# Performance work log

Measured on AMD Instinct MI355X. Metric: run time of the kernel, lower is better.

The kernel has to match this reference:

```python
import jax, jax.numpy as jnp
import numpy as np

N_DEPTH = 16  # == serialization_depth init kwarg


def _normalize(v, axis):
    # F.normalize: v / max(||v||, 1e-12)
    return v / jnp.maximum(jnp.linalg.norm(v, axis=axis, keepdims=True), 1e-12)


def _weighted_mean(p, mask):
    # p: [B,N,1], mask: [B,N]
    n = jnp.sum(mask, axis=1, keepdims=True)[..., None]
    return jnp.sum(p * mask[..., None], axis=1, keepdims=True) / (n + 1e-9)


def _select_duplet(points, m, k1, k2):
    # pick 2 random valid points (argmin of rand + big penalty on masked-out) and average
    B, N, _ = points.shape
    def pick(k):
        s = jax.random.uniform(k, (B, N)) + (1.0 - m) * 1e9
        idx = jnp.argmin(s, axis=1)           # [B]
        return jnp.take_along_axis(points, idx[:, None, None], axis=1)  # [B,1,3]
    return (pick(k1) + pick(k2)) * 0.5


def _align(points, ml, mr, ks):
    pl = points - _select_duplet(points, ml, ks[0], ks[1])
    pr = points - _select_duplet(points, mr, ks[2], ks[3])
    return pl * ml[..., None] + pr * mr[..., None]


def _serialize(coords, mask, n_depth, key):
    B, N, _ = coords.shape
    inf = float(2 ** (n_depth // 2 + 3))
    s0 = 2 ** (n_depth // 2 + 1)
    # integer halving each step, exactly like score_scale // 2 in torch
    scales = jnp.asarray(np.array([s0 >> i for i in range(n_depth)], dtype=np.float32))
    keys = jax.random.split(key, n_depth * 5).reshape(n_depth, 5)

    total0 = jnp.zeros((B, N, 1), coords.dtype)
    oldABC0 = jnp.ones((B, 3, 1), coords.dtype)

    def step(carry, inp):
        points, oldABC, total = carry
        ks, scale = inp
        ABC = jax.random.normal(ks[0], (B, 3, 1), coords.dtype)
        angle = jnp.sum(_normalize(ABC, 1) * _normalize(oldABC, 1), axis=1, keepdims=True)
        sgn = jnp.sign(angle)
        sgn = jnp.where(sgn == 0, 1.0, sgn)
        ABC = ABC * sgn
        proj = points @ ABC                    # [B,N,1]
        proj = proj - _weighted_mean(proj, mask)
        score = jnp.sign(proj)                 # [B,N,1]
        total = total + score * scale
        ml = jnp.minimum(jax.nn.relu(-score[..., 0]), mask)
        mr = jnp.minimum(jax.nn.relu(score[..., 0]), mask)
        points = _align(points, ml, mr, ks[1:])
        return (points, ABC, total), None

    (_, _, total), _ = jax.lax.scan(step, (coords, oldABC0, total0), (keys, scales))
    total = total + inf * (1.0 - mask)[..., None]
    return jnp.argsort(total[..., 0], axis=1)  # [B,N]


def setup_inputs() -> dict:
    key = jax.random.key(0)
    k1, k2 = jax.random.split(key)
    B, N, D = 16, 8192, 256
    x = jax.random.normal(k1, (B, N, D), dtype=jnp.float32)
    x_coords = jax.random.normal(k2, (B, N, 3), dtype=jnp.float32)
    mask = jnp.ones((B, N), dtype=jnp.float32)
    return {"x": x, "x_coords": x_coords, "mask": mask}


def reference(x, x_coords, mask):
    key = jax.random.key(42)
    idx = _serialize(x_coords, mask, N_DEPTH, key)   # [B,N] int
    # reverse_indices: gather(arange, idx) == idx, then argsort
    rev = jnp.argsort(idx, axis=1)
    x_out = jnp.take_along_axis(x, idx[:, :, None], axis=1)
    return x_out, rev
```

## Files before the change

kernel.cpp:

```cpp
#include <hip/hip_runtime.h>
#include <stdint.h>

#pragma clang fp contract(off)

constexpr bool kPartitionable = true;

constexpr int B_ = 16;
constexpr int N_ = 8192;
constexpr int TPB = 1024;

__device__ __forceinline__ void tf2x32(uint32_t k0, uint32_t k1,
                                       uint32_t x0, uint32_t x1,
                                       uint32_t& o0, uint32_t& o1) {
  uint32_t ks2 = k0 ^ k1 ^ 0x1BD11BDAu;
  x0 += k0; x1 += k1;
#define RND(r) { x0 += x1; x1 = (x1 << (r)) | (x1 >> (32 - (r))); x1 ^= x0; }
  RND(13) RND(15) RND(26) RND(6)   x0 += k1;  x1 += ks2 + 1u;
  RND(17) RND(29) RND(16) RND(24)  x0 += ks2; x1 += k0  + 2u;
  RND(13) RND(15) RND(26) RND(6)   x0 += k0;  x1 += k1  + 3u;
  RND(17) RND(29) RND(16) RND(24)  x0 += k1;  x1 += ks2 + 4u;
  RND(13) RND(15) RND(26) RND(6)   x0 += ks2; x1 += k0  + 5u;
#undef RND
  o0 = x0; o1 = x1;
}

__device__ __forceinline__ uint32_t rbits(uint32_t k0, uint32_t k1,
                                          uint32_t i, uint32_t half) {
  uint32_t o0, o1;
  if (kPartitionable) {
    tf2x32(k0, k1, 0u, i, o0, o1);
    return o0 ^ o1;
  } else {
    if (i < half) { tf2x32(k0, k1, i, half + i, o0, o1); return o0; }
    else          { tf2x32(k0, k1, i - half, i, o0, o1); return o1; }
  }
}

__device__ __forceinline__ void derive_key(uint32_t j, uint32_t& k0, uint32_t& k1) {
  uint32_t o0, o1;
  if (kPartitionable) {
    tf2x32(0u, 42u, 0u, j, o0, o1);
    k0 = o0; k1 = o1;
  } else {
    uint32_t a = 2u * j, b = 2u * j + 1u, t0, t1;
    if (a < 80u) { tf2x32(0u, 42u, a, 80u + a, t0, t1); k0 = t0; }
    else         { tf2x32(0u, 42u, a - 80u, a, t0, t1); k0 = t1; }
    if (b < 80u) { tf2x32(0u, 42u, b, 80u + b, t0, t1); k1 = t0; }
    else         { tf2x32(0u, 42u, b - 80u, b, t0, t1); k1 = t1; }
  }
}

__device__ __forceinline__ float u01_from_bits(uint32_t bits) {
  return __fsub_rn(__uint_as_float((bits >> 9) | 0x3f800000u), 1.0f);
}

__device__ __forceinline__ float xla_logf(float x) {
  uint32_t ix = __float_as_uint(x);
  int e = (int)((ix >> 23) & 0xffu) - 126;
  float m = __uint_as_float((ix & 0x007fffffu) | 0x3f000000u);
  float ef = (float)e;
  if (m < 0.707106781186547524f) {
    ef = __fsub_rn(ef, 1.0f);
    m = __fsub_rn(__fadd_rn(m, m), 1.0f);
  } else {
    m = __fsub_rn(m, 1.0f);
  }
  float z = __fmul_rn(m, m);
  float y = 7.0376836292e-2f;
  y = __fadd_rn(__fmul_rn(y, m), -1.1514610310e-1f);
  y = __fadd_rn(__fmul_rn(y, m),  1.1676998740e-1f);
  y = __fadd_rn(__fmul_rn(y, m), -1.2420140846e-1f);
  y = __fadd_rn(__fmul_rn(y, m),  1.4249322787e-1f);
  y = __fadd_rn(__fmul_rn(y, m), -1.6668057665e-1f);
  y = __fadd_rn(__fmul_rn(y, m),  2.0000714765e-1f);
  y = __fadd_rn(__fmul_rn(y, m), -2.4999993993e-1f);
  y = __fadd_rn(__fmul_rn(y, m),  3.3333331174e-1f);
  y = __fmul_rn(__fmul_rn(y, m), z);
  y = __fadd_rn(y, __fmul_rn(ef, -2.12194440e-4f));
  y = __fadd_rn(y, __fmul_rn(-0.5f, z));
  float r = __fadd_rn(m, y);
  r = __fadd_rn(r, __fmul_rn(ef, 0.693359375f));
  return r;
}

__device__ __forceinline__ float xla_log1p(float z) {
  if (fabsf(z) < 1e-4f)
    return __fmul_rn(__fadd_rn(__fmul_rn(-0.5f, z), 1.0f), z);
  return xla_logf(__fadd_rn(z, 1.0f));
}

__device__ __forceinline__ float erfinv_xla(float x) {
  float xx = __fmul_rn(x, x);
  float w = -xla_log1p(-xx);
  float p;
  if (w < 5.0f) {
    float ww = __fsub_rn(w, 2.5f);
    p = 2.81022636e-08f;
    p = __fadd_rn(__fmul_rn(p, ww),  3.43273939e-07f);
    p = __fadd_rn(__fmul_rn(p, ww), -3.5233877e-06f);
    p = __fadd_rn(__fmul_rn(p, ww), -4.39150654e-06f);
    p = __fadd_rn(__fmul_rn(p, ww),  0.00021858087f);
    p = __fadd_rn(__fmul_rn(p, ww), -0.00125372503f);
    p = __fadd_rn(__fmul_rn(p, ww), -0.00417768164f);
    p = __fadd_rn(__fmul_rn(p, ww),  0.246640727f);
    p = __fadd_rn(__fmul_rn(p, ww),  1.50140941f);
  } else {
    float ww = __fsub_rn(__fsqrt_rn(w), 3.0f);
    p = -0.000200214257f;
    p = __fadd_rn(__fmul_rn(p, ww),  0.000100950558f);
    p = __fadd_rn(__fmul_rn(p, ww),  0.00134934322f);
    p = __fadd_rn(__fmul_rn(p, ww), -0.00367342844f);
    p = __fadd_rn(__fmul_rn(p, ww),  0.00573950773f);
    p = __fadd_rn(__fmul_rn(p, ww), -0.0076224613f);
    p = __fadd_rn(__fmul_rn(p, ww),  0.00943887047f);
    p = __fadd_rn(__fmul_rn(p, ww),  1.00167406f);
    p = __fadd_rn(__fmul_rn(p, ww),  2.83297682f);
  }
  return __fmul_rn(p, x);
}

#define ACC4(v) { s = __fadd_rn(s, (v).x); s = __fadd_rn(s, (v).y); \
                  s = __fadd_rn(s, (v).z); s = __fadd_rn(s, (v).w); }

__device__ __forceinline__ float seq_sum_8192(const float4* v) {
  float4 a0=v[0],a1=v[1],a2=v[2],a3=v[3],a4=v[4],a5=v[5],a6=v[6],a7=v[7];
  float s = 0.f;
  for (int c = 0; c < 256; c += 2) {
    const int nb = (c + 1) << 3, na = (c + 2) << 3;
    float4 b0=v[nb+0],b1=v[nb+1],b2=v[nb+2],b3=v[nb+3];
    float4 b4=v[nb+4],b5=v[nb+5],b6=v[nb+6],b7=v[nb+7];
    ACC4(a0) ACC4(a1) ACC4(a2) ACC4(a3) ACC4(a4) ACC4(a5) ACC4(a6) ACC4(a7)
    a0=v[na+0];a1=v[na+1];a2=v[na+2];a3=v[na+3];
    a4=v[na+4];a5=v[na+5];a6=v[na+6];a7=v[na+7];
    ACC4(b0) ACC4(b1) ACC4(b2) ACC4(b3) ACC4(b4) ACC4(b5) ACC4(b6) ACC4(b7)
  }
  return s;
}

__global__ __launch_bounds__(TPB, 1)
void serialize_kernel(const float* __restrict__ coords, const float* __restrict__ mask,
                      float* __restrict__ pts_ws, int* __restrict__ idx_ws,
                      float* __restrict__ rev_out) {
  const int b = blockIdx.x;
  const int tid = threadIdx.x;

  __shared__ __align__(16) float pm[N_ + 32];
  __shared__ float    pv[4][16];
  __shared__ int      pi[4][16];
  __shared__ float    s_abcs[10][3], s_dl[3], s_dr[3];
  __shared__ float    s_stash[32];
  __shared__ float    s_mean, s_denom;
  __shared__ uint32_t s_k0[50], s_k1[50];

  float* pts = pts_ws + (size_t)b * N_ * 3;
  const float* cb = coords + (size_t)b * N_ * 3;
  const float* mb = mask + (size_t)b * N_;

  const float kLo = -0x1.fffffep-1f;
  const float kSqrt2 = 0x1.6a09e6p+0f;

  if (tid < 50) derive_key((uint32_t)tid, s_k0[tid], s_k1[tid]);

  float m_[8];
  {
    float4 m4a = *(const float4*)(mb + 4 * tid);
    float4 m4b = *(const float4*)(mb + 4096 + 4 * tid);
    m_[0]=m4a.x; m_[1]=m4a.y; m_[2]=m4a.z; m_[3]=m4a.w;
    m_[4]=m4b.x; m_[5]=m4b.y; m_[6]=m4b.z; m_[7]=m4b.w;
    ((float4*)pm)[tid] = m4a;
    ((float4*)pm)[1024 + tid] = m4b;
  }

  float p_[8][3];
  {
    const float4* cA = (const float4*)(cb + 12 * tid);
    const float4* cB = (const float4*)(cb + 12288 + 12 * tid);
    float4 v0=cA[0], v1=cA[1], v2=cA[2];
    p_[0][0]=v0.x; p_[0][1]=v0.y; p_[0][2]=v0.z;
    p_[1][0]=v0.w; p_[1][1]=v1.x; p_[1][2]=v1.y;
    p_[2][0]=v1.z; p_[2][1]=v1.w; p_[2][2]=v2.x;
    p_[3][0]=v2.y; p_[3][1]=v2.z; p_[3][2]=v2.w;
    float4 w0=cB[0], w1=cB[1], w2=cB[2];
    p_[4][0]=w0.x; p_[4][1]=w0.y; p_[4][2]=w0.z;
    p_[5][0]=w0.w; p_[5][1]=w1.x; p_[5][2]=w1.y;
    p_[6][0]=w1.z; p_[6][1]=w1.w; p_[6][2]=w2.x;
    p_[7][0]=w2.y; p_[7][1]=w2.z; p_[7][2]=w2.w;
    float4* dA = (float4*)(pts + 12 * tid);
    float4* dB = (float4*)(pts + 12288 + 12 * tid);
    dA[0]=v0; dA[1]=v1; dA[2]=v2;
    dB[0]=w0; dB[1]=w1; dB[2]=w2;
  }

  float tot_[8];
#pragma unroll
  for (int e = 0; e < 8; ++e) tot_[e] = 0.f;

  __syncthreads();

  if (tid == 0) {
    __builtin_amdgcn_s_setprio(1);
    float s = seq_sum_8192((const float4*)pm);
    __builtin_amdgcn_s_setprio(0);
    s_denom = __fadd_rn(s, 1e-9f);
  } else if (tid == 64) {
    float o0 = 1.f, o1 = 1.f, o2 = 1.f;
    for (int tt = 0; tt < 10; ++tt) {
      float a[3];
#pragma unroll
      for (int c = 0; c < 3; ++c) {
        uint32_t bits = rbits(s_k0[5*tt], s_k1[5*tt], (uint32_t)(b*3 + c), 24u);
        float f = u01_from_bits(bits);
        float u = __fadd_rn(__fmul_rn(f, 2.0f), kLo);
        u = fmaxf(kLo, u);
        a[c] = __fmul_rn(kSqrt2, erfinv_xla(u));
      }
      float na2 = __fadd_rn(__fadd_rn(__fmul_rn(a[0],a[0]),__fmul_rn(a[1],a[1])),__fmul_rn(a[2],a[2]));
      float no2 = __fadd_rn(__fadd_rn(__fmul_rn(o0,o0),__fmul_rn(o1,o1)),__fmul_rn(o2,o2));
      float nan_ = fmaxf(__fsqrt_rn(na2), 1e-12f);
      float non_ = fmaxf(__fsqrt_rn(no2), 1e-12f);
      float u0=__fdiv_rn(a[0],nan_), u1=__fdiv_rn(a[1],nan_), u2=__fdiv_rn(a[2],nan_);
      float v0=__fdiv_rn(o0,non_),  v1=__fdiv_rn(o1,non_),  v2=__fdiv_rn(o2,non_);
      float ang = __fadd_rn(__fadd_rn(__fmul_rn(u0,v0),__fmul_rn(u1,v1)),__fmul_rn(u2,v2));
      float sg = (ang > 0.f) ? 1.f : ((ang < 0.f) ? -1.f : 1.f);
      a[0]=__fmul_rn(a[0],sg); a[1]=__fmul_rn(a[1],sg); a[2]=__fmul_rn(a[2],sg);
      s_abcs[tt][0]=a[0]; s_abcs[tt][1]=a[1]; s_abcs[tt][2]=a[2];
      o0=a[0]; o1=a[1]; o2=a[2];
    }
  }
  __syncthreads();

  float proj_[8], sc_[8];

  for (int t = 0; t < 10; ++t) {
    const float A0 = s_abcs[t][0], A1 = s_abcs[t][1], A2 = s_abcs[t][2];

#pragma unroll
    for (int e = 0; e < 8; ++e)
      proj_[e] = __fadd_rn(__fadd_rn(__fmul_rn(p_[e][0], A0), __fmul_rn(p_[e][1], A1)),
                           __fmul_rn(p_[e][2], A2));
    {
      float4 w0, w1;
      w0.x=__fmul_rn(proj_[0],m_[0]); w0.y=__fmul_rn(proj_[1],m_[1]);
      w0.z=__fmul_rn(proj_[2],m_[2]); w0.w=__fmul_rn(proj_[3],m_[3]);
      w1.x=__fmul_rn(proj_[4],m_[4]); w1.y=__fmul_rn(proj_[5],m_[5]);
      w1.z=__fmul_rn(proj_[6],m_[6]); w1.w=__fmul_rn(proj_[7],m_[7]);
      ((float4*)pm)[tid] = w0;
      ((float4*)pm)[1024 + tid] = w1;
    }
    __syncthreads();

    if (tid == 0) {
#pragma unroll
      for (int e = 0; e < 8; ++e) {
        s_stash[e*3+0]=p_[e][0]; s_stash[e*3+1]=p_[e][1]; s_stash[e*3+2]=p_[e][2];
        s_stash[24+e]=tot_[e];
      }
      __builtin_amdgcn_s_setprio(1);
      float s = seq_sum_8192((const float4*)pm);
      __builtin_amdgcn_s_setprio(0);
      s_mean = __fdiv_rn(s, s_denom);
#pragma unroll
      for (int e = 0; e < 8; ++e) {
        p_[e][0]=s_stash[e*3+0]; p_[e][1]=s_stash[e*3+1]; p_[e][2]=s_stash[e*3+2];
        tot_[e]=s_stash[24+e];
      }
    }

    float f_[4][8];
#pragma unroll
    for (int q = 0; q < 4; ++q) {
      uint32_t kk0 = s_k0[5*t+1+q], kk1 = s_k1[5*t+1+q];
#pragma unroll
      for (int e = 0; e < 8; ++e) {
        int n = (e < 4) ? (4*tid + e) : (4096 + 4*tid + (e - 4));
        f_[q][e] = u01_from_bits(rbits(kk0, kk1, (uint32_t)(b*N_ + n), 65536u));
      }
    }
    __syncthreads();

    const float mean = s_mean;
    const float sca = (float)(512u >> t);
    float bv[4]; int bi_[4];
#pragma unroll
    for (int q = 0; q < 4; ++q) { bv[q] = 1e30f; bi_[q] = 0x7fffffff; }
#pragma unroll
    for (int e = 0; e < 8; ++e) {
      float d = __fsub_rn(proj_[e], mean);
      float s0 = (d > 0.f) ? 1.f : ((d < 0.f) ? -1.f : 0.f);
      sc_[e] = s0;
      tot_[e] = __fadd_rn(tot_[e], __fmul_rn(s0, sca));
      float mlv = fminf(fmaxf(-s0, 0.f), m_[e]);
      float mrv = fminf(fmaxf( s0, 0.f), m_[e]);
      int n = (e < 4) ? (4*tid + e) : (4096 + 4*tid + (e - 4));
#pragma unroll
      for (int q = 0; q < 4; ++q) {
        float meff = (q < 2) ? mlv : mrv;
        float val = __fadd_rn(f_[q][e], __fmul_rn(__fsub_rn(1.0f, meff), 1e9f));
        if (val < bv[q] || (val == bv[q] && n < bi_[q])) { bv[q] = val; bi_[q] = n; }
      }
    }
#pragma unroll
    for (int off = 32; off > 0; off >>= 1) {
#pragma unroll
      for (int q = 0; q < 4; ++q) {
        float vv = __shfl_xor(bv[q], off);
        int   ii = __shfl_xor(bi_[q], off);
        if (vv < bv[q] || (vv == bv[q] && ii < bi_[q])) { bv[q] = vv; bi_[q] = ii; }
      }
    }
    if ((tid & 63) == 0) {
      int w = tid >> 6;
#pragma unroll
      for (int q = 0; q < 4; ++q) { pv[q][w] = bv[q]; pi[q][w] = bi_[q]; }
    }
    __syncthreads();

    if (tid < 64) {
      int w = tid & 15, q = tid >> 4;
      float v = pv[q][w]; int i = pi[q][w];
#pragma unroll
      for (int off = 1; off < 16; off <<= 1) {
        float vv = __shfl_xor(v, off);
        int   ii = __shfl_xor(i, off);
        if (vv < v || (vv == v && ii < i)) { v = vv; i = ii; }
      }
      int g0 = __shfl(i, 0), g1 = __shfl(i, 16), g2 = __shfl(i, 32), g3 = __shfl(i, 48);
      if (tid == 0) {
#pragma unroll
        for (int c = 0; c < 3; ++c) {
          s_dl[c] = __fmul_rn(__fadd_rn(pts[g0*3+c], pts[g1*3+c]), 0.5f);
          s_dr[c] = __fmul_rn(__fadd_rn(pts[g2*3+c], pts[g3*3+c]), 0.5f);
        }
      }
    }
    __syncthreads();

    {
      float dl0=s_dl[0], dl1=s_dl[1], dl2=s_dl[2];
      float dr0=s_dr[0], dr1=s_dr[1], dr2=s_dr[2];
#pragma unroll
      for (int e = 0; e < 8; ++e) {
        float s0 = sc_[e];
        float mlv = fminf(fmaxf(-s0, 0.f), m_[e]);
        float mrv = fminf(fmaxf( s0, 0.f), m_[e]);
        p_[e][0] = __fadd_rn(__fmul_rn(__fsub_rn(p_[e][0], dl0), mlv),
                             __fmul_rn(__fsub_rn(p_[e][0], dr0), mrv));
        p_[e][1] = __fadd_rn(__fmul_rn(__fsub_rn(p_[e][1], dl1), mlv),
                             __fmul_rn(__fsub_rn(p_[e][1], dr1), mrv));
        p_[e][2] = __fadd_rn(__fmul_rn(__fsub_rn(p_[e][2], dl2), mlv),
                             __fmul_rn(__fsub_rn(p_[e][2], dr2), mrv));
      }
      float4 v0, v1, v2;
      v0.x=p_[0][0]; v0.y=p_[0][1]; v0.z=p_[0][2]; v0.w=p_[1][0];
      v1.x=p_[1][1]; v1.y=p_[1][2]; v1.z=p_[2][0]; v1.w=p_[2][1];
      v2.x=p_[2][2]; v2.y=p_[3][0]; v2.z=p_[3][1]; v2.w=p_[3][2];
      float4* dA = (float4*)(pts + 12 * tid);
      dA[0]=v0; dA[1]=v1; dA[2]=v2;
      v0.x=p_[4][0]; v0.y=p_[4][1]; v0.z=p_[4][2]; v0.w=p_[5][0];
      v1.x=p_[5][1]; v1.y=p_[5][2]; v1.z=p_[6][0]; v1.w=p_[6][1];
      v2.x=p_[6][2]; v2.y=p_[7][0]; v2.z=p_[7][1]; v2.w=p_[7][2];
      float4* dB = (float4*)(pts + 12288 + 12 * tid);
      dB[0]=v0; dB[1]=v1; dB[2]=v2;
    }
  }

  uint32_t* keys = reinterpret_cast<uint32_t*>(pm);
  {
    uint32_t kk_[8];
#pragma unroll
    for (int e = 0; e < 8; ++e) {
      int n = (e < 4) ? (4*tid + e) : (4096 + 4*tid + (e - 4));
      float tf = __fadd_rn(tot_[e], __fmul_rn(2048.0f, __fsub_rn(1.0f, m_[e])));
      int bin = (int)tf + 1023;
      bin = min(max(bin, 0), 4095);
      kk_[e] = ((uint32_t)bin << 13) | (uint32_t)n;
    }
    uint4 u0, u1;
    u0.x=kk_[0]; u0.y=kk_[1]; u0.z=kk_[2]; u0.w=kk_[3];
    u1.x=kk_[4]; u1.y=kk_[5]; u1.z=kk_[6]; u1.w=kk_[7];
    ((uint4*)keys)[tid] = u0;
    ((uint4*)keys)[1024 + tid] = u1;
  }
  for (uint32_t kk = 2; kk <= (uint32_t)N_; kk <<= 1) {
    for (uint32_t j = kk >> 1; j > 0; j >>= 1) {
      __syncthreads();
#pragma unroll
      for (int r = 0; r < 4; ++r) {
        int pidx = tid + (r << 10);
        int i = ((pidx & ~((int)j - 1)) << 1) | (pidx & ((int)j - 1));
        int l = i | (int)j;
        uint32_t a = keys[i], c2 = keys[l];
        bool up = ((i & (int)kk) == 0);
        if ((a > c2) == up) { keys[i] = c2; keys[l] = a; }
      }
    }
  }
  __syncthreads();
#pragma unroll
  for (int r = 0; r < 8; ++r) {
    int pos = tid + (r << 10);
    uint32_t key = keys[pos];
    int n = (int)(key & 8191u);
    idx_ws[b * N_ + pos] = n;
    rev_out[b * N_ + n] = (float)pos;
  }
}

__global__ __launch_bounds__(256)
void gather_kernel(const float* __restrict__ x, const int* __restrict__ idx_ws,
                   float* __restrict__ out) {
  int row = blockIdx.x * 4 + (threadIdx.x >> 6);
  int lane = threadIdx.x & 63;
  int b = row >> 13;
  int n = idx_ws[row];
  const float4* src = reinterpret_cast<const float4*>(x + ((size_t)(b * N_ + n)) * 256);
  float4* dst = reinterpret_cast<float4*>(out + (size_t)row * 256);
  dst[lane] = src[lane];
}

extern "C" void kernel_launch(void* const* d_in, const int* in_sizes, int n_in,
                              void* d_out, int out_size, void* d_ws, size_t ws_size,
                              hipStream_t stream) {
  const float* x      = (const float*)d_in[0];
  const float* coords = (const float*)d_in[1];
  const float* mask   = (const float*)d_in[2];
  float* out = (float*)d_out;
  float* pts_ws = (float*)d_ws;
  int*   idx_ws = (int*)((char*)d_ws + (size_t)B_ * N_ * 3 * sizeof(float));
  float* rev_out = out + (size_t)B_ * N_ * 256;

  serialize_kernel<<<dim3(B_), dim3(TPB), 0, stream>>>(coords, mask, pts_ws, idx_ws, rev_out);
  gather_kernel<<<dim3(B_ * N_ / 4), dim3(256), 0, stream>>>(x, idx_ws, out);
}
```

Before: 635.5 us.

## Precompute random uniforms and ABC vectors in a separate wide kernel

Moves the Threefry random generation for the argmin selection and the ABC direction vectors out of the 16-block serialize kernel into a new 641-block kernel, which writes them to workspace for serialize to load. This spreads the heavy hash work across the whole GPU instead of 16 CUs inside the serial loop. The mask denominator is now computed with a wave-shuffle reduction instead of a sequential single-thread sum. In exchange it adds a kernel launch and about 20 MB of global write plus read traffic. The parallel denominator sum may round differently from the sequential order used before.

```diff
diff --git a/kernel.cpp b/kernel.cpp
--- a/kernel.cpp
+++ b/kernel.cpp
@@ -8,6 +8,7 @@
 constexpr int B_ = 16;
 constexpr int N_ = 8192;
 constexpr int TPB = 1024;
+constexpr int NSTEP = 10;
 
 __device__ __forceinline__ void tf2x32(uint32_t k0, uint32_t k1,
                                        uint32_t x0, uint32_t x1,
@@ -24,30 +25,16 @@
   o0 = x0; o1 = x1;
 }
 
-__device__ __forceinline__ uint32_t rbits(uint32_t k0, uint32_t k1,
-                                          uint32_t i, uint32_t half) {
+__device__ __forceinline__ uint32_t rbits(uint32_t k0, uint32_t k1, uint32_t i) {
   uint32_t o0, o1;
-  if (kPartitionable) {
-    tf2x32(k0, k1, 0u, i, o0, o1);
-    return o0 ^ o1;
-  } else {
-    if (i < half) { tf2x32(k0, k1, i, half + i, o0, o1); return o0; }
-    else          { tf2x32(k0, k1, i - half, i, o0, o1); return o1; }
-  }
+  tf2x32(k0, k1, 0u, i, o0, o1);
+  return o0 ^ o1;
 }
 
 __device__ __forceinline__ void derive_key(uint32_t j, uint32_t& k0, uint32_t& k1) {
   uint32_t o0, o1;
-  if (kPartitionable) {
-    tf2x32(0u, 42u, 0u, j, o0, o1);
-    k0 = o0; k1 = o1;
-  } else {
-    uint32_t a = 2u * j, b = 2u * j + 1u, t0, t1;
-    if (a < 80u) { tf2x32(0u, 42u, a, 80u + a, t0, t1); k0 = t0; }
-    else         { tf2x32(0u, 42u, a - 80u, a, t0, t1); k0 = t1; }
-    if (b < 80u) { tf2x32(0u, 42u, b, 80u + b, t0, t1); k1 = t0; }
-    else         { tf2x32(0u, 42u, b - 80u, b, t0, t1); k1 = t1; }
-  }
+  tf2x32(0u, 42u, 0u, j, o0, o1);
+  k0 = o0; k1 = o1;
 }
 
 __device__ __forceinline__ float u01_from_bits(uint32_t bits) {
@@ -119,6 +106,60 @@
   return __fmul_rn(p, x);
 }
 
+__global__ __launch_bounds__(TPB)
+void rand_kernel(float* __restrict__ uni, float* __restrict__ abc) {
+  const int blk = blockIdx.x;
+  const int tid = threadIdx.x;
+  if (blk < 640) {
+    int b = blk / 40, r = blk % 40, t = r / 4, q = r % 4;
+    uint32_t k0, k1;
+    derive_key((uint32_t)(5 * t + 1 + q), k0, k1);
+    float* dst = uni + (((size_t)b * NSTEP + t) * 4 + q) * (size_t)N_;
+    float4 lo, hi;
+    int n0 = 4 * tid, n1 = 4096 + 4 * tid;
+    lo.x = u01_from_bits(rbits(k0, k1, (uint32_t)(b * N_ + n0 + 0)));
+    lo.y = u01_from_bits(rbits(k0, k1, (uint32_t)(b * N_ + n0 + 1)));
+    lo.z = u01_from_bits(rbits(k0, k1, (uint32_t)(b * N_ + n0 + 2)));
+    lo.w = u01_from_bits(rbits(k0, k1, (uint32_t)(b * N_ + n0 + 3)));
+    hi.x = u01_from_bits(rbits(k0, k1, (uint32_t)(b * N_ + n1 + 0)));
+    hi.y = u01_from_bits(rbits(k0, k1, (uint32_t)(b * N_ + n1 + 1)));
+    hi.z = u01_from_bits(rbits(k0, k1, (uint32_t)(b * N_ + n1 + 2)));
+    hi.w = u01_from_bits(rbits(k0, k1, (uint32_t)(b * N_ + n1 + 3)));
+    *(float4*)(dst + n0) = lo;
+    *(float4*)(dst + n1) = hi;
+  } else if (tid < 16) {
+    const int b = tid;
+    const float kLo = -0x1.fffffep-1f;
+    const float kSqrt2 = 0x1.6a09e6p+0f;
+    float o0 = 1.f, o1 = 1.f, o2 = 1.f;
+    for (int t = 0; t < NSTEP; ++t) {
+      uint32_t k0, k1;
+      derive_key((uint32_t)(5 * t), k0, k1);
+      float a[3];
+#pragma unroll
+      for (int c = 0; c < 3; ++c) {
+        float f = u01_from_bits(rbits(k0, k1, (uint32_t)(b * 3 + c)));
+        float u = __fadd_rn(__fmul_rn(f, 2.0f), kLo);
+        u = fmaxf(kLo, u);
+        a[c] = __fmul_rn(kSqrt2, erfinv_xla(u));
+      }
+      float na2 = __fadd_rn(__fadd_rn(__fmul_rn(a[0],a[0]),__fmul_rn(a[1],a[1])),__fmul_rn(a[2],a[2]));
+      float no2 = __fadd_rn(__fadd_rn(__fmul_rn(o0,o0),__fmul_rn(o1,o1)),__fmul_rn(o2,o2));
+      float nan_ = fmaxf(__fsqrt_rn(na2), 1e-12f);
+      float non_ = fmaxf(__fsqrt_rn(no2), 1e-12f);
+      float u0=__fdiv_rn(a[0],nan_), u1=__fdiv_rn(a[1],nan_), u2=__fdiv_rn(a[2],nan_);
+      float v0=__fdiv_rn(o0,non_),  v1=__fdiv_rn(o1,non_),  v2=__fdiv_rn(o2,non_);
+      float ang = __fadd_rn(__fadd_rn(__fmul_rn(u0,v0),__fmul_rn(u1,v1)),__fmul_rn(u2,v2));
+      float sg = (ang > 0.f) ? 1.f : ((ang < 0.f) ? -1.f : 1.f);
+      a[0]=__fmul_rn(a[0],sg); a[1]=__fmul_rn(a[1],sg); a[2]=__fmul_rn(a[2],sg);
+      abc[b * 30 + t * 3 + 0] = a[0];
+      abc[b * 30 + t * 3 + 1] = a[1];
+      abc[b * 30 + t * 3 + 2] = a[2];
+      o0 = a[0]; o1 = a[1]; o2 = a[2];
+    }
+  }
+}
+
 #define ACC4(v) { s = __fadd_rn(s, (v).x); s = __fadd_rn(s, (v).y); \
                   s = __fadd_rn(s, (v).z); s = __fadd_rn(s, (v).w); }
 
@@ -139,6 +180,7 @@
 
 __global__ __launch_bounds__(TPB, 1)
 void serialize_kernel(const float* __restrict__ coords, const float* __restrict__ mask,
+                      const float* __restrict__ uni, const float* __restrict__ abc,
                       float* __restrict__ pts_ws, int* __restrict__ idx_ws,
                       float* __restrict__ rev_out) {
   const int b = blockIdx.x;
@@ -147,19 +189,16 @@
   __shared__ __align__(16) float pm[N_ + 32];
   __shared__ float    pv[4][16];
   __shared__ int      pi[4][16];
-  __shared__ float    s_abcs[10][3], s_dl[3], s_dr[3];
-  __shared__ float    s_stash[32];
+  __shared__ float    s_abcs[NSTEP][3], s_dl[3], s_dr[3];
+  __shared__ float    s_stash[48];
+  __shared__ float    s_red[16];
   __shared__ float    s_mean, s_denom;
-  __shared__ uint32_t s_k0[50], s_k1[50];
 
   float* pts = pts_ws + (size_t)b * N_ * 3;
   const float* cb = coords + (size_t)b * N_ * 3;
   const float* mb = mask + (size_t)b * N_;
 
-  const float kLo = -0x1.fffffep-1f;
-  const float kSqrt2 = 0x1.6a09e6p+0f;
-
-  if (tid < 50) derive_key((uint32_t)tid, s_k0[tid], s_k1[tid]);
+  if (tid < 30) s_abcs[tid / 3][tid % 3] = abc[b * 30 + tid];
 
   float m_[8];
   {
@@ -167,8 +206,6 @@
     float4 m4b = *(const float4*)(mb + 4096 + 4 * tid);
     m_[0]=m4a.x; m_[1]=m4a.y; m_[2]=m4a.z; m_[3]=m4a.w;
     m_[4]=m4b.x; m_[5]=m4b.y; m_[6]=m4b.z; m_[7]=m4b.w;
-    ((float4*)pm)[tid] = m4a;
-    ((float4*)pm)[1024 + tid] = m4b;
   }
 
   float p_[8][3];
@@ -191,47 +228,31 @@
     dB[0]=w0; dB[1]=w1; dB[2]=w2;
   }
 
+  {
+    float ds = 0.f;
+#pragma unroll
+    for (int e = 0; e < 8; ++e) ds = __fadd_rn(ds, m_[e]);
+#pragma unroll
+    for (int off = 32; off > 0; off >>= 1) ds = __fadd_rn(ds, __shfl_xor(ds, off));
+    if ((tid & 63) == 0) s_red[tid >> 6] = ds;
+  }
+  __syncthreads();
+  if (tid == 0) {
+    float s = 0.f;
+#pragma unroll
+    for (int w = 0; w < 16; ++w) s = __fadd_rn(s, s_red[w]);
+    s_denom = __fadd_rn(s, 1e-9f);
+  }
+
   float tot_[8];
 #pragma unroll
   for (int e = 0; e < 8; ++e) tot_[e] = 0.f;
 
   __syncthreads();
 
-  if (tid == 0) {
-    __builtin_amdgcn_s_setprio(1);
-    float s = seq_sum_8192((const float4*)pm);
-    __builtin_amdgcn_s_setprio(0);
-    s_denom = __fadd_rn(s, 1e-9f);
-  } else if (tid == 64) {
-    float o0 = 1.f, o1 = 1.f, o2 = 1.f;
-    for (int tt = 0; tt < 10; ++tt) {
-      float a[3];
-#pragma unroll
-      for (int c = 0; c < 3; ++c) {
-        uint32_t bits = rbits(s_k0[5*tt], s_k1[5*tt], (uint32_t)(b*3 + c), 24u);
-        float f = u01_from_bits(bits);
-        float u = __fadd_rn(__fmul_rn(f, 2.0f), kLo);
-        u = fmaxf(kLo, u);
-        a[c] = __fmul_rn(kSqrt2, erfinv_xla(u));
-      }
-      float na2 = __fadd_rn(__fadd_rn(__fmul_rn(a[0],a[0]),__fmul_rn(a[1],a[1])),__fmul_rn(a[2],a[2]));
-      float no2 = __fadd_rn(__fadd_rn(__fmul_rn(o0,o0),__fmul_rn(o1,o1)),__fmul_rn(o2,o2));
-      float nan_ = fmaxf(__fsqrt_rn(na2), 1e-12f);
-      float non_ = fmaxf(__fsqrt_rn(no2), 1e-12f);
-      float u0=__fdiv_rn(a[0],nan_), u1=__fdiv_rn(a[1],nan_), u2=__fdiv_rn(a[2],nan_);
-      float v0=__fdiv_rn(o0,non_),  v1=__fdiv_rn(o1,non_),  v2=__fdiv_rn(o2,non_);
-      float ang = __fadd_rn(__fadd_rn(__fmul_rn(u0,v0),__fmul_rn(u1,v1)),__fmul_rn(u2,v2));
-      float sg = (ang > 0.f) ? 1.f : ((ang < 0.f) ? -1.f : 1.f);
-      a[0]=__fmul_rn(a[0],sg); a[1]=__fmul_rn(a[1],sg); a[2]=__fmul_rn(a[2],sg);
-      s_abcs[tt][0]=a[0]; s_abcs[tt][1]=a[1]; s_abcs[tt][2]=a[2];
-      o0=a[0]; o1=a[1]; o2=a[2];
-    }
-  }
-  __syncthreads();
-
   float proj_[8], sc_[8];
 
-  for (int t = 0; t < 10; ++t) {
+  for (int t = 0; t < NSTEP; ++t) {
     const float A0 = s_abcs[t][0], A1 = s_abcs[t][1], A2 = s_abcs[t][2];
 
 #pragma unroll
@@ -247,6 +268,16 @@
       ((float4*)pm)[tid] = w0;
       ((float4*)pm)[1024 + tid] = w1;
     }
+
+    float4 fl[4], fh[4];
+    {
+      const float* ub = uni + (((size_t)b * NSTEP + t) * 4) * (size_t)N_;
+#pragma unroll
+      for (int q = 0; q < 4; ++q) {
+        fl[q] = *(const float4*)(ub + (size_t)q * N_ + 4 * tid);
+        fh[q] = *(const float4*)(ub + (size_t)q * N_ + 4096 + 4 * tid);
+      }
+    }
     __syncthreads();
 
     if (tid == 0) {
@@ -254,6 +285,8 @@
       for (int e = 0; e < 8; ++e) {
         s_stash[e*3+0]=p_[e][0]; s_stash[e*3+1]=p_[e][1]; s_stash[e*3+2]=p_[e][2];
         s_stash[24+e]=tot_[e];
+        s_stash[32+e]=proj_[e];
+        s_stash[40+e]=m_[e];
       }
       __builtin_amdgcn_s_setprio(1);
       float s = seq_sum_8192((const float4*)pm);
@@ -263,17 +296,8 @@
       for (int e = 0; e < 8; ++e) {
         p_[e][0]=s_stash[e*3+0]; p_[e][1]=s_stash[e*3+1]; p_[e][2]=s_stash[e*3+2];
         tot_[e]=s_stash[24+e];
-      }
-    }
-
-    float f_[4][8];
-#pragma unroll
-    for (int q = 0; q < 4; ++q) {
-      uint32_t kk0 = s_k0[5*t+1+q], kk1 = s_k1[5*t+1+q];
-#pragma unroll
-      for (int e = 0; e < 8; ++e) {
-        int n = (e < 4) ? (4*tid + e) : (4096 + 4*tid + (e - 4));
-        f_[q][e] = u01_from_bits(rbits(kk0, kk1, (uint32_t)(b*N_ + n), 65536u));
+        proj_[e]=s_stash[32+e];
+        m_[e]=s_stash[40+e];
       }
     }
     __syncthreads();
@@ -295,7 +319,10 @@
 #pragma unroll
       for (int q = 0; q < 4; ++q) {
         float meff = (q < 2) ? mlv : mrv;
-        float val = __fadd_rn(f_[q][e], __fmul_rn(__fsub_rn(1.0f, meff), 1e9f));
+        float fval;
+        if (e < 4) fval = (e == 0 ? fl[q].x : e == 1 ? fl[q].y : e == 2 ? fl[q].z : fl[q].w);
+        else       fval = (e == 4 ? fh[q].x : e == 5 ? fh[q].y : e == 6 ? fh[q].z : fh[q].w);
+        float val = __fadd_rn(fval, __fmul_rn(__fsub_rn(1.0f, meff), 1e9f));
         if (val < bv[q] || (val == bv[q] && n < bi_[q])) { bv[q] = val; bi_[q] = n; }
       }
     }
@@ -425,10 +452,15 @@
   const float* coords = (const float*)d_in[1];
   const float* mask   = (const float*)d_in[2];
   float* out = (float*)d_out;
-  float* pts_ws = (float*)d_ws;
-  int*   idx_ws = (int*)((char*)d_ws + (size_t)B_ * N_ * 3 * sizeof(float));
+
+  float* uni    = (float*)d_ws;
+  float* abc    = uni + (size_t)B_ * NSTEP * 4 * N_;
+  float* pts_ws = abc + 480;
+  int*   idx_ws = (int*)(pts_ws + (size_t)B_ * N_ * 3);
   float* rev_out = out + (size_t)B_ * N_ * 256;
 
-  serialize_kernel<<<dim3(B_), dim3(TPB), 0, stream>>>(coords, mask, pts_ws, idx_ws, rev_out);
+  rand_kernel<<<dim3(641), dim3(TPB), 0, stream>>>(uni, abc);
+  serialize_kernel<<<dim3(B_), dim3(TPB), 0, stream>>>(coords, mask, uni, abc,
+                                                       pts_ws, idx_ws, rev_out);
   gather_kernel<<<dim3(B_ * N_ / 4), dim3(256), 0, stream>>>(x, idx_ws, out);
 }
```

Measured after the change: 546.8 us. 1.16x faster.
